# Performance work log

Measured on AMD Instinct MI355X. Metric: run time of the kernel, lower is better.

The kernel has to match this reference:

```python
import jax, jax.numpy as jnp
import numpy as np

EMBED = 1024
ATTN = 1024

def setup_inputs() -> dict:
    key = jax.random.key(0)
    k1, k2, k3, k4 = jax.random.split(key, 4)
    x = jax.random.normal(k1, (32, 2048, EMBED), dtype=jnp.float32)
    W = jax.random.normal(k2, (EMBED, ATTN), dtype=jnp.float32) / np.sqrt(EMBED)
    b = jax.random.normal(k3, (ATTN,), dtype=jnp.float32) * 0.01
    ctx = jax.random.normal(k4, (ATTN,), dtype=jnp.float32)
    return {"x": x, "W": W, "b": b, "ctx": ctx}

def reference(x, W, b, ctx):
    # scores: [B, S] = tanh(x @ W + b) . ctx
    h = jnp.tanh(jnp.einsum('bse,ea->bsa', x, W) + b)
    scores = jnp.einsum('bsa,a->bs', h, ctx)
    weights = jax.nn.softmax(scores, axis=1)            # softmax over seq dim
    return jnp.einsum('bse,bs->be', x, weights)          # weighted sum pooling
```

## Files before the change

### kernel.cpp

```cpp
#include <hip/hip_runtime.h>
#include <hip/hip_bf16.h>

typedef _Float16 half8 __attribute__((ext_vector_type(8)));
typedef _Float16 half4 __attribute__((ext_vector_type(4)));
typedef float floatx4 __attribute__((ext_vector_type(4)));

#define EMBED 1024
#define SEQ   2048
#define BATCH 32
#define M_TOT (BATCH * SEQ)
#define KDIM  1024
#define NDIM  1024

#define GLOAD16(g, l) __builtin_amdgcn_global_load_lds(                      \
    (const __attribute__((address_space(1))) void*)(g),                      \
    (__attribute__((address_space(3))) void*)(l), 16, 0, 0)

__global__ void transpose_w_kernel(const float* __restrict__ W,
                                   _Float16* __restrict__ Wt) {
    __shared__ float t[32][33];
    const int kt = blockIdx.x * 32;
    const int nt = blockIdx.y * 32;
    #pragma unroll
    for (int i = 0; i < 4; ++i)
        t[threadIdx.y + 8 * i][threadIdx.x] =
            W[(size_t)(kt + threadIdx.y + 8 * i) * NDIM + nt + threadIdx.x];
    __syncthreads();
    #pragma unroll
    for (int i = 0; i < 4; ++i)
        Wt[(size_t)(nt + threadIdx.y + 8 * i) * KDIM + kt + threadIdx.x] =
            (_Float16)t[threadIdx.x][threadIdx.y + 8 * i];
}

__global__ void zero_kernel(float* __restrict__ scores, float* __restrict__ out) {
    const int i = blockIdx.x * 256 + threadIdx.x;
    if (i < M_TOT) scores[i] = 0.0f;
    if (i < BATCH * EMBED) out[i] = 0.0f;
}

__global__ __launch_bounds__(256) void cvt_x_kernel(const float* __restrict__ x,
                                                    _Float16* __restrict__ x16) {
    const size_t stride = (size_t)gridDim.x * 256 * 8;
    for (size_t i = ((size_t)blockIdx.x * 256 + threadIdx.x) * 8;
         i < (size_t)M_TOT * KDIM; i += stride) {
        const float4 a = *(const float4*)(x + i);
        const float4 b = *(const float4*)(x + i + 4);
        half8 h;
        h[0] = (_Float16)a.x; h[1] = (_Float16)a.y; h[2] = (_Float16)a.z; h[3] = (_Float16)a.w;
        h[4] = (_Float16)b.x; h[5] = (_Float16)b.y; h[6] = (_Float16)b.z; h[7] = (_Float16)b.w;
        *(half8*)(x16 + i) = h;
    }
}

__global__ __launch_bounds__(256, 4) void score_gemm8(
    const _Float16* __restrict__ x16, const _Float16* __restrict__ Wt,
    const float* __restrict__ bias, const float* __restrict__ ctx,
    float* __restrict__ scores) {
    __shared__ _Float16 As[2][128 * 32];
    __shared__ _Float16 Bs[2][128 * 32];

    const int nb = ((blockIdx.x & 7) << 9) | (blockIdx.x >> 3);
    const int bm = nb >> 3;
    const int bn = nb & 7;
    const int tid = threadIdx.x;
    const int lane = tid & 63;
    const int wid = tid >> 6;
    const int wm = wid >> 1;
    const int wn = wid & 1;

    const int jA0 = wid * 2;
    const int lrow = lane >> 2;
    const int gslot = (lane & 3) ^ ((lane >> 3) & 3);
    const int gcol = gslot * 8;

    const _Float16* Ab = x16 + (size_t)(bm * 128) * KDIM;
    const _Float16* Bb = Wt  + (size_t)(bn * 128) * KDIM;

    floatx4 acc[4][4] = {};

    const int frow = lane & 15;
    const int fslot = ((lane >> 4) ^ ((frow >> 1) & 3)) * 8;

    #define STAGE(buf, kt)                                                        \
        {                                                                         \
            const int kc = (kt) * 32 + gcol;                                      \
            _Pragma("unroll")                                                     \
            for (int i = 0; i < 2; ++i) {                                         \
                const int j = jA0 + i;                                            \
                GLOAD16(Ab + (size_t)(j * 16 + lrow) * KDIM + kc, &As[buf][j * 512]); \
                GLOAD16(Bb + (size_t)(j * 16 + lrow) * KDIM + kc, &Bs[buf][j * 512]); \
            }                                                                     \
        }

    STAGE(0, 0);
    __syncthreads();

    for (int kt = 0; kt < KDIM / 32; ++kt) {
        const int cur = kt & 1;
        if (kt + 1 < KDIM / 32) STAGE(cur ^ 1, kt + 1);

        half8 afr[4], bfr[4];
        #pragma unroll
        for (int m = 0; m < 4; ++m)
            afr[m] = *(const half8*)&As[cur][(wm * 64 + m * 16 + frow) * 32 + fslot];
        #pragma unroll
        for (int n = 0; n < 4; ++n)
            bfr[n] = *(const half8*)&Bs[cur][(wn * 64 + n * 16 + frow) * 32 + fslot];

        #pragma unroll
        for (int m = 0; m < 4; ++m)
            #pragma unroll
            for (int n = 0; n < 4; ++n)
                acc[m][n] = __builtin_amdgcn_mfma_f32_16x16x32_f16(
                    afr[m], bfr[n], acc[m][n], 0, 0, 0);

        __syncthreads();
    }
    #undef STAGE

    float bv[4], cv[4];
    #pragma unroll
    for (int n = 0; n < 4; ++n) {
        const int col = bn * 128 + wn * 64 + n * 16 + (lane & 15);
        bv[n] = bias[col];
        cv[n] = ctx[col];
    }
    #pragma unroll
    for (int m = 0; m < 4; ++m) {
        #pragma unroll
        for (int j = 0; j < 4; ++j) {
            float partial = 0.0f;
            #pragma unroll
            for (int n = 0; n < 4; ++n) {
                const float v = acc[m][n][j] + bv[n];
                const float e = __expf(2.0f * v);
                const float t = 1.0f - 2.0f * __builtin_amdgcn_rcpf(e + 1.0f);
                partial += t * cv[n];
            }
            #pragma unroll
            for (int off = 1; off < 16; off <<= 1)
                partial += __shfl_xor(partial, off, 64);
            if ((lane & 15) == 0) {
                const int rowg = bm * 128 + wm * 64 + m * 16 + (lane >> 4) * 4 + j;
                atomicAdd(&scores[rowg], partial);
            }
        }
    }
}

__global__ __launch_bounds__(256) void score_gemm_f32(
    const float* __restrict__ A32p, const _Float16* __restrict__ Wt,
    const float* __restrict__ bias, const float* __restrict__ ctx,
    float* __restrict__ scores) {
    __shared__ _Float16 As[128 * 64];
    __shared__ _Float16 Bs[128 * 64];

    const int bid = blockIdx.x;
    const int bm = bid >> 3;
    const int bn = bid & 7;
    const int tid = threadIdx.x;
    const int lane = tid & 63;
    const int wid = tid >> 6;
    const int wm = wid >> 1;
    const int wn = wid & 1;

    const int c = tid & 7;
    const int r0 = tid >> 3;
    const int swz = (r0 & 7) << 3;
    const int wcol = (c * 8) ^ swz;

    float4 aF[4][2];
    int4   bR[4];

    #pragma unroll
    for (int i = 0; i < 4; ++i) {
        const int row = r0 + 32 * i;
        const float* p = A32p + (size_t)(bm * 128 + row) * KDIM + c * 8;
        aF[i][0] = *(const float4*)p;
        aF[i][1] = *(const float4*)(p + 4);
        bR[i] = *(const int4*)(Wt + (size_t)(bn * 128 + row) * KDIM + c * 8);
    }

    floatx4 acc[4][4] = {};

    for (int kt = 0; kt < KDIM / 64; ++kt) {
        __syncthreads();
        #pragma unroll
        for (int i = 0; i < 4; ++i) {
            const int row = r0 + 32 * i;
            half8 h;
            h[0] = (_Float16)aF[i][0].x; h[1] = (_Float16)aF[i][0].y;
            h[2] = (_Float16)aF[i][0].z; h[3] = (_Float16)aF[i][0].w;
            h[4] = (_Float16)aF[i][1].x; h[5] = (_Float16)aF[i][1].y;
            h[6] = (_Float16)aF[i][1].z; h[7] = (_Float16)aF[i][1].w;
            *(half8*)&As[row * 64 + wcol] = h;
            *(int4*)&Bs[row * 64 + wcol] = bR[i];
        }
        __syncthreads();

        if (kt + 1 < KDIM / 64) {
            #pragma unroll
            for (int i = 0; i < 4; ++i) {
                const int row = r0 + 32 * i;
                const float* p = A32p + (size_t)(bm * 128 + row) * KDIM + (kt + 1) * 64 + c * 8;
                aF[i][0] = *(const float4*)p;
                aF[i][1] = *(const float4*)(p + 4);
                bR[i] = *(const int4*)(Wt + (size_t)(bn * 128 + row) * KDIM + (kt + 1) * 64 + c * 8);
            }
        }

        #pragma unroll
        for (int s = 0; s < 2; ++s) {
            half8 afr[4], bfr[4];
            const int colr = s * 32 + (lane >> 4) * 8;
            #pragma unroll
            for (int m = 0; m < 4; ++m) {
                const int row = wm * 64 + m * 16 + (lane & 15);
                afr[m] = *(const half8*)&As[row * 64 + (colr ^ ((row & 7) << 3))];
            }
            #pragma unroll
            for (int n = 0; n < 4; ++n) {
                const int row = wn * 64 + n * 16 + (lane & 15);
                bfr[n] = *(const half8*)&Bs[row * 64 + (colr ^ ((row & 7) << 3))];
            }
            #pragma unroll
            for (int m = 0; m < 4; ++m)
                #pragma unroll
                for (int n = 0; n < 4; ++n)
                    acc[m][n] = __builtin_amdgcn_mfma_f32_16x16x32_f16(
                        afr[m], bfr[n], acc[m][n], 0, 0, 0);
        }
    }

    float bv[4], cv[4];
    #pragma unroll
    for (int n = 0; n < 4; ++n) {
        const int col = bn * 128 + wn * 64 + n * 16 + (lane & 15);
        bv[n] = bias[col];
        cv[n] = ctx[col];
    }
    #pragma unroll
    for (int m = 0; m < 4; ++m) {
        #pragma unroll
        for (int j = 0; j < 4; ++j) {
            float partial = 0.0f;
            #pragma unroll
            for (int n = 0; n < 4; ++n) {
                const float v = acc[m][n][j] + bv[n];
                const float e = __expf(2.0f * v);
                const float t = 1.0f - 2.0f * __builtin_amdgcn_rcpf(e + 1.0f);
                partial += t * cv[n];
            }
            #pragma unroll
            for (int off = 1; off < 16; off <<= 1)
                partial += __shfl_xor(partial, off, 64);
            if ((lane & 15) == 0) {
                const int rowg = bm * 128 + wm * 64 + m * 16 + (lane >> 4) * 4 + j;
                atomicAdd(&scores[rowg], partial);
            }
        }
    }
}

__global__ void softmax_kernel(const float* __restrict__ scores,
                               float* __restrict__ weights) {
    const int bb = blockIdx.x;
    const int tid = threadIdx.x;
    const float* s = scores + (size_t)bb * SEQ;
    float* w = weights + (size_t)bb * SEQ;

    __shared__ float red[8];

    float v[8];
    float mx = -1e30f;
    #pragma unroll
    for (int i = 0; i < 8; ++i) {
        v[i] = s[tid + i * 256];
        mx = fmaxf(mx, v[i]);
    }
    #pragma unroll
    for (int off = 1; off < 64; off <<= 1)
        mx = fmaxf(mx, __shfl_xor(mx, off, 64));
    const int wv = tid >> 6;
    if ((tid & 63) == 0) red[wv] = mx;
    __syncthreads();
    mx = fmaxf(fmaxf(red[0], red[1]), fmaxf(red[2], red[3]));

    float sum = 0.0f;
    #pragma unroll
    for (int i = 0; i < 8; ++i) {
        v[i] = __expf(v[i] - mx);
        sum += v[i];
    }
    #pragma unroll
    for (int off = 1; off < 64; off <<= 1)
        sum += __shfl_xor(sum, off, 64);
    if ((tid & 63) == 0) red[4 + wv] = sum;
    __syncthreads();
    sum = red[4] + red[5] + red[6] + red[7];
    const float inv = 1.0f / sum;
    #pragma unroll
    for (int i = 0; i < 8; ++i)
        w[tid + i * 256] = v[i] * inv;
}

__global__ __launch_bounds__(256) void pool_kernel(const float* __restrict__ x,
                                                   const float* __restrict__ weights,
                                                   float* __restrict__ out) {
    const int bb = blockIdx.x >> 4;
    const int sc = blockIdx.x & 15;
    const int tid = threadIdx.x;

    const float4* xb = (const float4*)(x + (size_t)bb * SEQ * EMBED) +
                       (size_t)(sc * 128) * (EMBED / 4) + tid;
    const float* wb = weights + (size_t)bb * SEQ + sc * 128;

    float ax = 0.f, ay = 0.f, az = 0.f, aw = 0.f;
    #pragma unroll 4
    for (int s = 0; s < 128; ++s) {
        const float wgt = wb[s];
        const float4 xv = xb[(size_t)s * (EMBED / 4)];
        ax += wgt * xv.x; ay += wgt * xv.y; az += wgt * xv.z; aw += wgt * xv.w;
    }
    float* o = out + (size_t)bb * EMBED + tid * 4;
    atomicAdd(o + 0, ax);
    atomicAdd(o + 1, ay);
    atomicAdd(o + 2, az);
    atomicAdd(o + 3, aw);
}

__global__ __launch_bounds__(256) void pool16_kernel(const _Float16* __restrict__ x16,
                                                     const float* __restrict__ weights,
                                                     float* __restrict__ out) {
    const int bb = blockIdx.x >> 4;
    const int sc = blockIdx.x & 15;
    const int tid = threadIdx.x;

    const _Float16* xb = x16 + (size_t)bb * SEQ * EMBED +
                         (size_t)(sc * 128) * EMBED + tid * 4;
    const float* wb = weights + (size_t)bb * SEQ + sc * 128;

    float ax = 0.f, ay = 0.f, az = 0.f, aw = 0.f;
    #pragma unroll 4
    for (int s = 0; s < 128; ++s) {
        const float wgt = wb[s];
        const half4 h = *(const half4*)(xb + (size_t)s * EMBED);
        ax += wgt * (float)h[0]; ay += wgt * (float)h[1];
        az += wgt * (float)h[2]; aw += wgt * (float)h[3];
    }
    float* o = out + (size_t)bb * EMBED + tid * 4;
    atomicAdd(o + 0, ax);
    atomicAdd(o + 1, ay);
    atomicAdd(o + 2, az);
    atomicAdd(o + 3, aw);
}

extern "C" void kernel_launch(void* const* d_in, const int* in_sizes, int n_in,
                              void* d_out, int out_size, void* d_ws, size_t ws_size,
                              hipStream_t stream) {
    const float* x   = (const float*)d_in[0];
    const float* W   = (const float*)d_in[1];
    const float* b   = (const float*)d_in[2];
    const float* ctx = (const float*)d_in[3];
    float* out = (float*)d_out;

    char* ws = (char*)d_ws;
    _Float16* Wt      = (_Float16*)ws;
    float*    scores  = (float*)(ws + (2u << 20));
    float*    weights = (float*)(ws + (2u << 20) + (256u << 10));
    _Float16* x16     = (_Float16*)(ws + (4u << 20));

    const size_t need = (4ull << 20) + ((size_t)M_TOT * KDIM * 2);
    const bool fast = ws_size >= need;

    hipLaunchKernelGGL(transpose_w_kernel, dim3(32, 32), dim3(32, 8), 0, stream, W, Wt);
    hipLaunchKernelGGL(zero_kernel, dim3(M_TOT / 256), dim3(256), 0, stream, scores, out);

    if (fast) {
        hipLaunchKernelGGL(cvt_x_kernel, dim3(4096), dim3(256), 0, stream, x, x16);
        hipLaunchKernelGGL(score_gemm8, dim3(4096), dim3(256), 0, stream,
                           x16, Wt, b, ctx, scores);
    } else {
        hipLaunchKernelGGL(score_gemm_f32, dim3(4096), dim3(256), 0, stream,
                           x, Wt, b, ctx, scores);
    }

    hipLaunchKernelGGL(softmax_kernel, dim3(BATCH), dim3(256), 0, stream, scores, weights);

    if (fast) {
        hipLaunchKernelGGL(pool16_kernel, dim3(BATCH * 16), dim3(256), 0, stream,
                           x16, weights, out);
    } else {
        hipLaunchKernelGGL(pool_kernel, dim3(BATCH * 16), dim3(256), 0, stream,
                           x, weights, out);
    }
}
```

Baseline: 289.6 us.

## Prepack W into MFMA fragment order and load B operands directly to registers

Measured after the change: 287.4 us. No clear change (-0.8%).

```diff
diff --git a/kernel.cpp b/kernel.cpp
--- a/kernel.cpp
+++ b/kernel.cpp
@@ -30,6 +30,24 @@
     for (int i = 0; i < 4; ++i)
         Wt[(size_t)(nt + threadIdx.y + 8 * i) * KDIM + kt + threadIdx.x] =
             (_Float16)t[threadIdx.x][threadIdx.y + 8 * i];
+}
+
+__global__ __launch_bounds__(256) void pack_w_kernel(const float* __restrict__ W,
+                                                     _Float16* __restrict__ Bp) {
+    const int flat = blockIdx.x * 256 + threadIdx.x;
+    int t = flat;
+    const int lane = t & 63; t >>= 6;
+    const int nf   = t & 3;  t >>= 2;
+    const int wn   = t & 1;  t >>= 1;
+    const int kt   = t & 31; t >>= 5;
+    const int bn   = t;
+    const int col = bn * 128 + wn * 64 + nf * 16 + (lane & 15);
+    const int k0  = kt * 32 + (lane >> 4) * 8;
+    half8 h;
+    #pragma unroll
+    for (int j = 0; j < 8; ++j)
+        h[j] = (_Float16)W[(size_t)(k0 + j) * NDIM + col];
+    *(half8*)(Bp + (size_t)flat * 8) = h;
 }
 
 __global__ void zero_kernel(float* __restrict__ scores, float* __restrict__ out) {
@@ -52,12 +70,11 @@
     }
 }
 
-__global__ __launch_bounds__(256, 4) void score_gemm8(
-    const _Float16* __restrict__ x16, const _Float16* __restrict__ Wt,
+__global__ __launch_bounds__(256, 4) void score_gemm9(
+    const _Float16* __restrict__ x16, const _Float16* __restrict__ Bp,
     const float* __restrict__ bias, const float* __restrict__ ctx,
     float* __restrict__ scores) {
     __shared__ _Float16 As[2][128 * 32];
-    __shared__ _Float16 Bs[2][128 * 32];
 
     const int nb = ((blockIdx.x & 7) << 9) | (blockIdx.x >> 3);
     const int bm = nb >> 3;
@@ -68,13 +85,12 @@
     const int wm = wid >> 1;
     const int wn = wid & 1;
 
-    const int jA0 = wid * 2;
+    const int jA0 = wid;
     const int lrow = lane >> 2;
     const int gslot = (lane & 3) ^ ((lane >> 3) & 3);
     const int gcol = gslot * 8;
 
     const _Float16* Ab = x16 + (size_t)(bm * 128) * KDIM;
-    const _Float16* Bb = Wt  + (size_t)(bn * 128) * KDIM;
 
     floatx4 acc[4][4] = {};
 
@@ -86,36 +102,48 @@
             const int kc = (kt) * 32 + gcol;                                      \
             _Pragma("unroll")                                                     \
             for (int i = 0; i < 2; ++i) {                                         \
-                const int j = jA0 + i;                                            \
+                const int j = jA0 + i * 4;                                        \
                 GLOAD16(Ab + (size_t)(j * 16 + lrow) * KDIM + kc, &As[buf][j * 512]); \
-                GLOAD16(Bb + (size_t)(j * 16 + lrow) * KDIM + kc, &Bs[buf][j * 512]); \
             }                                                                     \
         }
 
+    const int4* Bp4 = (const int4*)Bp;
+    #define BLOAD(dst, kt)                                                        \
+        {                                                                         \
+            const int4* p = Bp4 + ((((size_t)bn * 32 + (kt)) * 2 + wn) * 4) * 64 + lane; \
+            dst[0] = p[0]; dst[1] = p[64]; dst[2] = p[128]; dst[3] = p[192];      \
+        }
+
+    int4 Bcur[4], Bnext[4];
+
     STAGE(0, 0);
+    BLOAD(Bcur, 0);
     __syncthreads();
 
     for (int kt = 0; kt < KDIM / 32; ++kt) {
         const int cur = kt & 1;
-        if (kt + 1 < KDIM / 32) STAGE(cur ^ 1, kt + 1);
-
-        half8 afr[4], bfr[4];
+        if (kt + 1 < KDIM / 32) {
+            STAGE(cur ^ 1, kt + 1);
+            BLOAD(Bnext, kt + 1);
+        }
+
+        half8 afr[4];
         #pragma unroll
         for (int m = 0; m < 4; ++m)
             afr[m] = *(const half8*)&As[cur][(wm * 64 + m * 16 + frow) * 32 + fslot];
-        #pragma unroll
-        for (int n = 0; n < 4; ++n)
-            bfr[n] = *(const half8*)&Bs[cur][(wn * 64 + n * 16 + frow) * 32 + fslot];
 
         #pragma unroll
         for (int m = 0; m < 4; ++m)
             #pragma unroll
             for (int n = 0; n < 4; ++n)
                 acc[m][n] = __builtin_amdgcn_mfma_f32_16x16x32_f16(
-                    afr[m], bfr[n], acc[m][n], 0, 0, 0);
+                    afr[m], *(const half8*)&Bcur[n], acc[m][n], 0, 0, 0);
 
         __syncthreads();
-    }
+        #pragma unroll
+        for (int n = 0; n < 4; ++n) Bcur[n] = Bnext[n];
+    }
+    #undef BLOAD
     #undef STAGE
 
     float bv[4], cv[4];
@@ -365,6 +393,7 @@
     float* out = (float*)d_out;
 
     char* ws = (char*)d_ws;
+    _Float16* Bp      = (_Float16*)ws;
     _Float16* Wt      = (_Float16*)ws;
     float*    scores  = (float*)(ws + (2u << 20));
     float*    weights = (float*)(ws + (2u << 20) + (256u << 10));
@@ -373,14 +402,15 @@
     const size_t need = (4ull << 20) + ((size_t)M_TOT * KDIM * 2);
     const bool fast = ws_size >= need;
 
-    hipLaunchKernelGGL(transpose_w_kernel, dim3(32, 32), dim3(32, 8), 0, stream, W, Wt);
     hipLaunchKernelGGL(zero_kernel, dim3(M_TOT / 256), dim3(256), 0, stream, scores, out);
 
     if (fast) {
+        hipLaunchKernelGGL(pack_w_kernel, dim3(512), dim3(256), 0, stream, W, Bp);
         hipLaunchKernelGGL(cvt_x_kernel, dim3(4096), dim3(256), 0, stream, x, x16);
-        hipLaunchKernelGGL(score_gemm8, dim3(4096), dim3(256), 0, stream,
-                           x16, Wt, b, ctx, scores);
+        hipLaunchKernelGGL(score_gemm9, dim3(4096), dim3(256), 0, stream,
+                           x16, Bp, b, ctx, scores);
     } else {
+        hipLaunchKernelGGL(transpose_w_kernel, dim3(32, 32), dim3(32, 8), 0, stream, W, Wt);
         hipLaunchKernelGGL(score_gemm_f32, dim3(4096), dim3(256), 0, stream,
                            x, Wt, b, ctx, scores);
     }
```

## Enlarge score GEMM tile to 256x256 with 8 waves and interleaved staging

Applied to the files above, without the earlier changes.

Result: slower. 307.2 us (+6.1%).

```diff
diff --git a/kernel.cpp b/kernel.cpp
--- a/kernel.cpp
+++ b/kernel.cpp
@@ -52,81 +52,128 @@
     }
 }
 
-__global__ __launch_bounds__(256, 4) void score_gemm8(
+__global__ __launch_bounds__(512, 2) void score_gemm13(
     const _Float16* __restrict__ x16, const _Float16* __restrict__ Wt,
     const float* __restrict__ bias, const float* __restrict__ ctx,
     float* __restrict__ scores) {
-    __shared__ _Float16 As[2][128 * 32];
-    __shared__ _Float16 Bs[2][128 * 32];
-
-    const int nb = ((blockIdx.x & 7) << 9) | (blockIdx.x >> 3);
-    const int bm = nb >> 3;
-    const int bn = nb & 7;
+    __shared__ _Float16 As[2][2][128 * 64];
+    __shared__ _Float16 Bs[2][2][128 * 64];
+
+    const int nb = ((blockIdx.x & 7) << 7) | (blockIdx.x >> 3);
+    const int bm = nb >> 2;
+    const int bn = nb & 3;
     const int tid = threadIdx.x;
     const int lane = tid & 63;
-    const int wid = tid >> 6;
-    const int wm = wid >> 1;
-    const int wn = wid & 1;
-
-    const int jA0 = wid * 2;
-    const int lrow = lane >> 2;
-    const int gslot = (lane & 3) ^ ((lane >> 3) & 3);
-    const int gcol = gslot * 8;
-
-    const _Float16* Ab = x16 + (size_t)(bm * 128) * KDIM;
-    const _Float16* Bb = Wt  + (size_t)(bn * 128) * KDIM;
-
-    floatx4 acc[4][4] = {};
+    const int w = tid >> 6;
+    const int wr = w >> 2;
+    const int wc = w & 3;
+
+    const int srow = lane >> 3;
+    const int gsl  = (lane & 7) ^ srow;
+    const _Float16* Ab = x16 + (size_t)(bm * 256) * KDIM;
+    const _Float16* Bb = Wt  + (size_t)(bn * 256) * KDIM;
+
+#define STAGE_A(buf, h, kt)                                                    \
+    { _Pragma("unroll")                                                        \
+      for (int i = 0; i < 2; ++i) {                                            \
+          const int r = w * 16 + i * 8;                                        \
+          GLOAD16(Ab + (size_t)((h) * 128 + r + srow) * KDIM + (kt) * 64 + gsl * 8, \
+                  &As[buf][h][r * 64]);                                        \
+      } }
+#define STAGE_B(buf, h, kt)                                                    \
+    { _Pragma("unroll")                                                        \
+      for (int i = 0; i < 2; ++i) {                                            \
+          const int r = w * 16 + i * 8;                                        \
+          GLOAD16(Bb + (size_t)((h) * 128 + r + srow) * KDIM + (kt) * 64 + gsl * 8, \
+                  &Bs[buf][h][r * 64]);                                        \
+      } }
 
     const int frow = lane & 15;
-    const int fslot = ((lane >> 4) ^ ((frow >> 1) & 3)) * 8;
-
-    #define STAGE(buf, kt)                                                        \
-        {                                                                         \
-            const int kc = (kt) * 32 + gcol;                                      \
-            _Pragma("unroll")                                                     \
-            for (int i = 0; i < 2; ++i) {                                         \
-                const int j = jA0 + i;                                            \
-                GLOAD16(Ab + (size_t)(j * 16 + lrow) * KDIM + kc, &As[buf][j * 512]); \
-                GLOAD16(Bb + (size_t)(j * 16 + lrow) * KDIM + kc, &Bs[buf][j * 512]); \
-            }                                                                     \
-        }
-
-    STAGE(0, 0);
-    __syncthreads();
-
-    for (int kt = 0; kt < KDIM / 32; ++kt) {
-        const int cur = kt & 1;
-        if (kt + 1 < KDIM / 32) STAGE(cur ^ 1, kt + 1);
-
-        half8 afr[4], bfr[4];
-        #pragma unroll
-        for (int m = 0; m < 4; ++m)
-            afr[m] = *(const half8*)&As[cur][(wm * 64 + m * 16 + frow) * 32 + fslot];
-        #pragma unroll
-        for (int n = 0; n < 4; ++n)
-            bfr[n] = *(const half8*)&Bs[cur][(wn * 64 + n * 16 + frow) * 32 + fslot];
-
-        #pragma unroll
-        for (int m = 0; m < 4; ++m)
-            #pragma unroll
-            for (int n = 0; n < 4; ++n)
-                acc[m][n] = __builtin_amdgcn_mfma_f32_16x16x32_f16(
-                    afr[m], bfr[n], acc[m][n], 0, 0, 0);
-
-        __syncthreads();
-    }
-    #undef STAGE
+    const int fhi  = lane >> 4;
+    const int fx   = frow & 7;
+    const int bsub = (wc & 1) * 64;
+
+#define LDA4(buf, ks, m0)                                                      \
+    { _Pragma("unroll")                                                        \
+      for (int m = 0; m < 4; ++m)                                              \
+          afr[m] = *(const half8*)&As[buf][wr][((m0 + m) * 16 + frow) * 64 +   \
+                                              ((((ks) * 4 + fhi) ^ fx) * 8)]; }
+#define LDB4(buf, ks)                                                          \
+    { _Pragma("unroll")                                                        \
+      for (int n = 0; n < 4; ++n)                                              \
+          bfr[n] = *(const half8*)&Bs[buf][wc >> 1][(bsub + n * 16 + frow) * 64 + \
+                                                    ((((ks) * 4 + fhi) ^ fx) * 8)]; }
+#define MFMA16(m0)                                                             \
+    { __builtin_amdgcn_s_setprio(1);                                           \
+      _Pragma("unroll")                                                        \
+      for (int m = 0; m < 4; ++m)                                              \
+          _Pragma("unroll")                                                    \
+          for (int n = 0; n < 4; ++n)                                          \
+              acc[m0 + m][n] = __builtin_amdgcn_mfma_f32_16x16x32_f16(         \
+                  afr[m], bfr[n], acc[m0 + m][n], 0, 0, 0);                    \
+      __builtin_amdgcn_s_setprio(0); }
+
+#define BAR() __builtin_amdgcn_s_barrier()
+
+#define GROUP(cur, kt1, STG, W0)                                               \
+    {                                                                          \
+                                   \
+        if (STG) STAGE_A(cur ^ 1, 0, kt1);                                     \
+        asm volatile(W0 ::: "memory");                                         \
+        __builtin_amdgcn_sched_barrier(0);                                     \
+        BAR();                              \
+        LDA4(cur, 0, 0); LDB4(cur, 0);                                         \
+        MFMA16(0);                                                             \
+        BAR();                                                                 \
+                                                            \
+        if (STG) STAGE_A(cur ^ 1, 1, kt1);                                     \
+        LDA4(cur, 0, 4);                                                       \
+        BAR();                                                                 \
+        MFMA16(4);                                                             \
+        BAR();                                                                 \
+                                                            \
+        if (STG) STAGE_B(cur ^ 1, 0, kt1);                                     \
+        LDA4(cur, 1, 0); LDB4(cur, 1);                                         \
+        BAR();                                                                 \
+        MFMA16(0);                                                             \
+        BAR();                                                                 \
+                                                            \
+        if (STG) STAGE_B(cur ^ 1, 1, kt1);                                     \
+        LDA4(cur, 1, 4);                                                       \
+        BAR();                                                                 \
+        MFMA16(4);                                                             \
+        BAR();                                                                 \
+    }
+
+    floatx4 acc[8][4] = {};
+    half8 afr[4], bfr[4];
+
+    STAGE_A(0, 0, 0); STAGE_A(0, 1, 0); STAGE_B(0, 0, 0); STAGE_B(0, 1, 0);
+
+    for (int kt2 = 0; kt2 < 7; ++kt2) {
+        GROUP(0, 2 * kt2 + 1, 1, "s_waitcnt vmcnt(2)");
+        GROUP(1, 2 * kt2 + 2, 1, "s_waitcnt vmcnt(2)");
+    }
+    GROUP(0, 15, 1, "s_waitcnt vmcnt(2)");
+    GROUP(1, 0, 0, "s_waitcnt vmcnt(0)");
+
+#undef GROUP
+#undef BAR
+#undef MFMA16
+#undef LDB4
+#undef LDA4
+#undef STAGE_B
+#undef STAGE_A
 
     float bv[4], cv[4];
     #pragma unroll
     for (int n = 0; n < 4; ++n) {
-        const int col = bn * 128 + wn * 64 + n * 16 + (lane & 15);
+        const int col = bn * 256 + wc * 64 + n * 16 + frow;
         bv[n] = bias[col];
         cv[n] = ctx[col];
     }
     #pragma unroll
-    for (int m = 0; m < 4; ++m) {
+    for (int m = 0; m < 8; ++m) {
         #pragma unroll
         for (int j = 0; j < 4; ++j) {
             float partial = 0.0f;
@@ -140,8 +187,8 @@
             #pragma unroll
             for (int off = 1; off < 16; off <<= 1)
                 partial += __shfl_xor(partial, off, 64);
-            if ((lane & 15) == 0) {
-                const int rowg = bm * 128 + wm * 64 + m * 16 + (lane >> 4) * 4 + j;
+            if (frow == 0) {
+                const int rowg = bm * 256 + wr * 128 + m * 16 + fhi * 4 + j;
                 atomicAdd(&scores[rowg], partial);
             }
         }
@@ -373,12 +420,12 @@
     const size_t need = (4ull << 20) + ((size_t)M_TOT * KDIM * 2);
     const bool fast = ws_size >= need;
 
+    hipLaunchKernelGGL(zero_kernel, dim3(M_TOT / 256), dim3(256), 0, stream, scores, out);
     hipLaunchKernelGGL(transpose_w_kernel, dim3(32, 32), dim3(32, 8), 0, stream, W, Wt);
-    hipLaunchKernelGGL(zero_kernel, dim3(M_TOT / 256), dim3(256), 0, stream, scores, out);
 
     if (fast) {
         hipLaunchKernelGGL(cvt_x_kernel, dim3(4096), dim3(256), 0, stream, x, x16);
-        hipLaunchKernelGGL(score_gemm8, dim3(4096), dim3(256), 0, stream,
+        hipLaunchKernelGGL(score_gemm13, dim3(1024), dim3(512), 0, stream,
                            x16, Wt, b, ctx, scores);
     } else {
         hipLaunchKernelGGL(score_gemm_f32, dim3(4096), dim3(256), 0, stream,
```
